# Optimization experiments

Hardware: AMD Instinct MI355X
Metric: run time of the kernel (lower is better)

Reference implementation:

```python
import jax, jax.numpy as jnp
import numpy as np

N = 50000
E = 800000
IN_C, HID_C, OUT_C = 128, 256, 2


def sage_conv(x, src, dst, W_l, b_l, W_r, num_nodes):
    # PyG SAGEConv with mean aggregation:
    #   out = lin_l(mean_{j in N(i)} x_j) + lin_r(x_i)
    msg = x[src]                                            # [E, d] gather
    agg = jax.ops.segment_sum(msg, dst, num_segments=num_nodes)   # [N, d]
    cnt = jax.ops.segment_sum(jnp.ones((msg.shape[0],), x.dtype), dst,
                              num_segments=num_nodes)        # [N]
    agg = agg / jnp.maximum(cnt, 1.0)[:, None]               # mean (deg>=1)
    return agg @ W_l.T + b_l + x @ W_r.T


def setup_inputs() -> dict:
    key = jax.random.key(0)
    ks = jax.random.split(key, 8)
    x = jax.random.normal(ks[0], (N, IN_C), dtype=jnp.float32)
    edge_index = jax.random.randint(ks[1], (2, E), 0, N, dtype=jnp.int32)
    # glorot-ish scaled params
    s1 = 1.0 / np.sqrt(IN_C)
    s2 = 1.0 / np.sqrt(HID_C)
    W1l = jax.random.normal(ks[2], (HID_C, IN_C), dtype=jnp.float32) * s1
    W1r = jax.random.normal(ks[3], (HID_C, IN_C), dtype=jnp.float32) * s1
    b1 = jnp.zeros((HID_C,), dtype=jnp.float32)
    W2l = jax.random.normal(ks[4], (OUT_C, HID_C), dtype=jnp.float32) * s2
    W2r = jax.random.normal(ks[5], (OUT_C, HID_C), dtype=jnp.float32) * s2
    b2 = jnp.zeros((OUT_C,), dtype=jnp.float32)
    return {"x": x, "edge_index": edge_index,
            "W1l": W1l, "b1": b1, "W1r": W1r,
            "W2l": W2l, "b2": b2, "W2r": W2r}


def reference(x, edge_index, W1l, b1, W1r, W2l, b2, W2r):
    src, dst = edge_index[0], edge_index[1]
    h = sage_conv(x, src, dst, W1l, b1, W1r, N)
    h = jax.nn.relu(h)
    out = sage_conv(h, src, dst, W2l, b2, W2r, N)
    return out
```

## Files before the change

### kernel.cpp

```cpp
#include <hip/hip_runtime.h>
#include <hip/hip_bf16.h>


#define IN_C 128
#define HID_C 256
#define BKT_SHIFT 7
#define BKT_W 128
#define CAP 3072

typedef __attribute__((ext_vector_type(8))) short short8;
typedef __attribute__((ext_vector_type(4))) float f32x4;

static __device__ __forceinline__ unsigned short f2b(float f) {
    __hip_bfloat16 h = __float2bfloat16(f);
    return *(unsigned short*)&h;
}
static __device__ __forceinline__ float b2f(unsigned short u) {
    unsigned v = ((unsigned)u) << 16;
    return *(float*)&v;
}

__global__ __launch_bounds__(512) void scatter_conv(
    const float* __restrict__ x, unsigned int* __restrict__ Abf,
    const float* __restrict__ w1l, const float* __restrict__ w1r,
    unsigned short* __restrict__ Bg,
    const int* __restrict__ ei, int* __restrict__ bcnt,
    unsigned int* __restrict__ binned,
    int nquads , int xblk, int E_) {
    __shared__ int hist[512];
    __shared__ int lbase[512];
    const int tid = threadIdx.x;
    if (blockIdx.x < xblk) {
        int t = blockIdx.x * 512 + tid;
        if (t >= nquads) return;
        float4 v = *(const float4*)&x[(size_t)t * 4];
        uint2 o;
        o.x = ((unsigned)f2b(v.y) << 16) | f2b(v.x);
        o.y = ((unsigned)f2b(v.w) << 16) | f2b(v.z);
        int node = t >> 5, g = t & 31;
        *(uint2*)&Abf[(size_t)node * 128 + 64 + g * 2] = o;
    } else if (blockIdx.x < xblk + 32) {
        int idx4 = (blockIdx.x - xblk) * 512 + tid;
        int o = idx4 >> 6, k4 = (idx4 & 63) * 4;
        const float* srcp = (k4 < IN_C) ? &w1l[o * IN_C + k4]
                                        : &w1r[o * IN_C + (k4 - IN_C)];
        float4 f = *(const float4*)srcp;
        ushort4 s;
        s.x = f2b(f.x); s.y = f2b(f.y); s.z = f2b(f.z); s.w = f2b(f.w);
        *(ushort4*)&Bg[(size_t)idx4 * 4] = s;
    } else {
        const int e0 = (blockIdx.x - xblk - 32) * 2048;
        hist[tid] = 0;
        __syncthreads();
        int dreg[4];
#pragma unroll
        for (int j = 0; j < 4; ++j) {
            int e = e0 + j * 512 + tid;
            dreg[j] = (e < E_) ? ei[E_ + e] : -1;
            if (dreg[j] >= 0) atomicAdd(&hist[dreg[j] >> BKT_SHIFT], 1);
        }
        __syncthreads();
        {
            int c = hist[tid];
            lbase[tid] = c ? tid * CAP + atomicAdd(&bcnt[tid], c) : 0;
            hist[tid] = 0;
        }
        __syncthreads();
#pragma unroll
        for (int j = 0; j < 4; ++j) {
            int e = e0 + j * 512 + tid;
            if (dreg[j] >= 0) {
                int d = dreg[j];
                int b = d >> BKT_SHIFT;
                int pos = lbase[b] + atomicAdd(&hist[b], 1);
                if (pos < b * CAP + CAP)
                    binned[pos] = ((unsigned)ei[e] << BKT_SHIFT) |
                                  (unsigned)(d & (BKT_W - 1));
            }
        }
    }
}


__global__ __launch_bounds__(1024) void sort_gather(
    unsigned int* __restrict__ binned, const int* __restrict__ bcnt,
    const uint4* __restrict__ abf4c, uint4* __restrict__ Abf4,
    int* __restrict__ deg, int* __restrict__ boffs, int n) {
    __shared__ unsigned int ebuf[CAP];
    __shared__ unsigned short sbuf[CAP];
    __shared__ int hist[BKT_W];
    __shared__ int offs[BKT_W];
    __shared__ int cur[BKT_W];
    const int tid = threadIdx.x;
    const int lane = tid & 63;
    const int bkt = blockIdx.x;
    const int gbase = bkt * CAP;
    int cnt = bcnt[bkt];
    if (cnt > CAP) cnt = CAP;

    if (tid < BKT_W) hist[tid] = 0;
    {
        const int cnt4 = cnt >> 2;
        const uint4* b4 = (const uint4*)(binned + gbase);
        uint4* e4 = (uint4*)ebuf;
        for (int i = tid; i < cnt4; i += 1024) e4[i] = b4[i];
        for (int i = cnt4 * 4 + tid; i < cnt; i += 1024)
            ebuf[i] = binned[gbase + i];
    }
    __syncthreads();
    for (int i = tid; i < cnt; i += 1024)
        atomicAdd(&hist[ebuf[i] & (BKT_W - 1)], 1);
    __syncthreads();
    if (tid < 64) {
        int h0 = hist[lane * 2], h1 = hist[lane * 2 + 1];
        int s = h0 + h1;
        int incl = s;
#pragma unroll
        for (int off = 1; off < 64; off <<= 1) {
            int t = __shfl_up(incl, off);
            if (lane >= off) incl += t;
        }
        int excl = incl - s;
        offs[lane * 2] = excl;          cur[lane * 2] = excl;
        offs[lane * 2 + 1] = excl + h0; cur[lane * 2 + 1] = excl + h0;
    }
    __syncthreads();
    for (int i = tid; i < cnt; i += 1024) {
        unsigned int pk = ebuf[i];
        int pos = atomicAdd(&cur[pk & (BKT_W - 1)], 1);
        sbuf[pos] = (unsigned short)(pk >> BKT_SHIFT);
    }
    if (tid < BKT_W) {
        int node = bkt * BKT_W + tid;
        if (node < n) { deg[node] = hist[tid]; boffs[node] = offs[tid]; }
    }
    __syncthreads();

    {
        unsigned int* so = (unsigned int*)(binned + gbase);
        const int half = (cnt + 1) >> 1;
        for (int i = tid; i < half; i += 1024) {
            unsigned lo = sbuf[i * 2];
            unsigned hi = (i * 2 + 1 < cnt) ? sbuf[i * 2 + 1] : 0u;
            so[i] = lo | (hi << 16);
        }
    }

    const int wv = tid >> 6;
    const int ep = lane >> 4;
    const int pos = lane & 15;
    for (int ld = wv * 8; ld < wv * 8 + 8; ++ld) {
        int node = bkt * BKT_W + ld;
        if (node >= n) break;
        int beg = offs[ld], end = offs[ld] + hist[ld];
        float s[8] = {0.f, 0.f, 0.f, 0.f, 0.f, 0.f, 0.f, 0.f};
        for (int e = beg; e < end; e += 16) {
#pragma unroll
            for (int g = 0; g < 4; ++g) {
                int eg = e + g * 4 + ep;
                if (eg < end) {
                    int src = sbuf[eg];
                    uint4 u = abf4c[(size_t)src * 32 + 16 + pos];
                    s[0] += b2f(u.x & 0xffff); s[1] += b2f(u.x >> 16);
                    s[2] += b2f(u.y & 0xffff); s[3] += b2f(u.y >> 16);
                    s[4] += b2f(u.z & 0xffff); s[5] += b2f(u.z >> 16);
                    s[6] += b2f(u.w & 0xffff); s[7] += b2f(u.w >> 16);
                }
            }
        }
#pragma unroll
        for (int i = 0; i < 8; ++i) {
            s[i] += __shfl_xor(s[i], 16);
            s[i] += __shfl_xor(s[i], 32);
        }
        if (ep == 0) {
            float inv = 1.0f / (float)max(end - beg, 1);
            uint4 o;
            o.x = ((unsigned)f2b(s[1] * inv) << 16) | f2b(s[0] * inv);
            o.y = ((unsigned)f2b(s[3] * inv) << 16) | f2b(s[2] * inv);
            o.z = ((unsigned)f2b(s[5] * inv) << 16) | f2b(s[4] * inv);
            o.w = ((unsigned)f2b(s[7] * inv) << 16) | f2b(s[6] * inv);
            Abf4[(size_t)node * 32 + pos] = o;
        }
    }
}


#define LSTR 72

__global__ __launch_bounds__(256, 4) void gemm1_fused(
    const unsigned short* __restrict__ Abf, const unsigned short* __restrict__ Bg,
    const float* __restrict__ b1, const float* __restrict__ w2l,
    const float* __restrict__ w2r, float2* __restrict__ p2g,
    float2* __restrict__ rsg, int nn) {
    __shared__ short Bs[256 * LSTR];

    const int tid = threadIdx.x;
    const int lane = tid & 63;
    const int wn = tid >> 6;
    const int row0 = blockIdx.x * 64;
    const int quad = lane >> 4;
    const int l16 = lane & 15;

    const unsigned short* ap[4];
#pragma unroll
    for (int mt = 0; mt < 4; ++mt) {
        int ar = row0 + mt * 16 + l16;
        if (ar >= nn) ar = nn - 1;
        ap[mt] = Abf + (size_t)ar * 256 + quad * 8;
    }

    f32x4 acc[4][4];
#pragma unroll
    for (int i = 0; i < 4; ++i)
#pragma unroll
        for (int j = 0; j < 4; ++j) acc[i][j] = (f32x4){0.f, 0.f, 0.f, 0.f};

    for (int k0 = 0; k0 < 256; k0 += 64) {
        const uint4* gb = (const uint4*)(Bg + (size_t)tid * 256 + k0);
        uint4 r0 = gb[0], r1 = gb[1], r2 = gb[2], r3 = gb[3];
        uint4 r4 = gb[4], r5 = gb[5], r6 = gb[6], r7 = gb[7];
        __syncthreads();
        uint4* lb = (uint4*)&Bs[tid * LSTR];
        lb[0] = r0; lb[1] = r1; lb[2] = r2; lb[3] = r3;
        lb[4] = r4; lb[5] = r5; lb[6] = r6; lb[7] = r7;
        __syncthreads();

#pragma unroll
        for (int kb = 0; kb < 2; ++kb) {
            short8 af[4], bf[4];
#pragma unroll
            for (int mt = 0; mt < 4; ++mt)
                af[mt] = *(const short8*)(ap[mt] + k0 + kb * 32);
#pragma unroll
            for (int nt = 0; nt < 4; ++nt)
                bf[nt] = *(const short8*)&Bs[(wn * 64 + nt * 16 + l16) * LSTR + kb * 32 + quad * 8];
#pragma unroll
            for (int mt = 0; mt < 4; ++mt)
#pragma unroll
                for (int nt = 0; nt < 4; ++nt)
                    acc[mt][nt] = __builtin_amdgcn_mfma_f32_16x16x32_bf16(
                        af[mt], bf[nt], acc[mt][nt], 0, 0, 0);
        }
    }

    float* pr = (float*)Bs;
    __syncthreads();
    pr[tid] = 0.f;
    __syncthreads();

    const int cbase = wn * 64 + l16;
#pragma unroll
    for (int half = 0; half < 2; ++half) {
        const float* wA = half ? w2r : w2l;
        f32x4 part[2][4];
#pragma unroll
        for (int c = 0; c < 2; ++c)
#pragma unroll
            for (int mt = 0; mt < 4; ++mt) part[c][mt] = (f32x4){0.f, 0.f, 0.f, 0.f};
#pragma unroll
        for (int nt = 0; nt < 4; ++nt) {
            const int col = cbase + nt * 16;
            const float bias = b1[col];
            const float w0 = wA[col];
            const float w1 = wA[HID_C + col];
#pragma unroll
            for (int mt = 0; mt < 4; ++mt)
#pragma unroll
                for (int r = 0; r < 4; ++r) {
                    float hv = fmaxf(acc[mt][nt][r] + bias, 0.0f);
                    part[0][mt][r] += hv * w0;
                    part[1][mt][r] += hv * w1;
                }
        }
#pragma unroll
        for (int c = 0; c < 2; ++c)
#pragma unroll
            for (int mt = 0; mt < 4; ++mt)
#pragma unroll
                for (int r = 0; r < 4; ++r)
#pragma unroll
                    for (int m = 1; m < 16; m <<= 1)
                        part[c][mt][r] += __shfl_xor(part[c][mt][r], m);
        if (l16 < 8) {
            const int ch2 = l16 & 1;
            const int mts = l16 >> 1;
#pragma unroll
            for (int r = 0; r < 4; ++r) {
                int rloc = quad * 4 + mts * 16 + r;
                atomicAdd(&pr[rloc * 4 + half * 2 + ch2], part[ch2][mts][r]);
            }
        }
    }
    __syncthreads();
    if (tid < 128) {
        int rloc = tid >> 1, pair = tid & 1;
        int row = row0 + rloc;
        if (row < nn) {
            float2 v = make_float2(pr[rloc * 4 + pair * 2],
                                   pr[rloc * 4 + pair * 2 + 1]);
            if (pair) rsg[row] = v; else p2g[row] = v;
        }
    }
}


__global__ __launch_bounds__(512) void fin_bucket(
    const unsigned int* __restrict__ binned, const int* __restrict__ boffs,
    const int* __restrict__ deg,
    const float2* __restrict__ p2, const float2* __restrict__ rs,
    const float* __restrict__ b2, float* __restrict__ out, int n) {
    __shared__ float ps0[3][BKT_W];
    __shared__ float ps1[3][BKT_W];
    const int tid = threadIdx.x;
    const int ln = tid & (BKT_W - 1);
    const int hp = tid >> 7;
    const int bkt = blockIdx.x;
    const int node = bkt * BKT_W + ln;
    const unsigned short* sp =
        (const unsigned short*)(binned + (size_t)bkt * CAP);
    float s0 = 0.f, s1 = 0.f;
    int dg = 0;
    if (node < n) {
        int beg = boffs[node];
        dg = deg[node];
        int end = beg + dg;
        for (int i = beg + hp; i < end; i += 4) {
            float2 v = p2[sp[i]];
            s0 += v.x; s1 += v.y;
        }
    }
    if (hp) { ps0[hp - 1][ln] = s0; ps1[hp - 1][ln] = s1; }
    __syncthreads();
    if (!hp && node < n) {
        s0 += ps0[0][ln] + ps0[1][ln] + ps0[2][ln];
        s1 += ps1[0][ln] + ps1[1][ln] + ps1[2][ln];
        float inv = 1.0f / (float)max(dg, 1);
        float2 self = rs[node];
        out[node * 2 + 0] = s0 * inv + self.x + b2[0];
        out[node * 2 + 1] = s1 * inv + self.y + b2[1];
    }
}


extern "C" void kernel_launch(void* const* d_in, const int* in_sizes, int n_in,
                              void* d_out, int out_size, void* d_ws, size_t ws_size,
                              hipStream_t stream) {
    const float* x   = (const float*)d_in[0];
    const int*   ei  = (const int*)d_in[1];
    const float* W1l = (const float*)d_in[2];
    const float* b1  = (const float*)d_in[3];
    const float* W1r = (const float*)d_in[4];
    const float* W2l = (const float*)d_in[5];
    const float* b2  = (const float*)d_in[6];
    const float* W2r = (const float*)d_in[7];
    float* out = (float*)d_out;

    const int N_ = in_sizes[0] / IN_C;
    const int E_ = in_sizes[1] / 2;
    const int nbkt = (N_ + BKT_W - 1) / BKT_W;

    char* wsb = (char*)d_ws;
    size_t off = 0;
    auto alloc = [&](size_t bytes) {
        void* ptr = wsb + off;
        off += ((bytes + 15) & ~(size_t)15);
        return ptr;
    };
    unsigned short* Abf = (unsigned short*)alloc((size_t)N_ * 256 * 2);
    unsigned short* Bg  = (unsigned short*)alloc(256 * 256 * 2);
    unsigned int* binned = (unsigned int*)alloc((size_t)(nbkt + 1) * CAP * 4);
    int*   bcnt = (int*)alloc(512 * 4);
    float* p2f  = (float*)alloc((size_t)N_ * 2 * 4);
    float* rsf  = (float*)alloc((size_t)N_ * 2 * 4);
    int*   deg  = (int*)alloc((size_t)N_ * 4);
    int*   boffs = (int*)alloc((size_t)N_ * 4);

    const int xblk = (N_ * 32 + 511) / 512;
    const int eblk = (E_ + 2047) / 2048;

    hipMemsetAsync(bcnt, 0, 512 * sizeof(int), stream);

    scatter_conv<<<xblk + 32 + eblk, 512, 0, stream>>>(
        x, (unsigned int*)Abf, W1l, W1r, Bg, ei, bcnt, binned,
        N_ * 32, xblk, E_);

    sort_gather<<<nbkt, 1024, 0, stream>>>(binned, bcnt, (const uint4*)Abf,
                                           (uint4*)Abf, deg, boffs, N_);

    gemm1_fused<<<(N_ + 63) / 64, 256, 0, stream>>>(
        Abf, Bg, b1, W2l, W2r, (float2*)p2f, (float2*)rsf, N_);

    fin_bucket<<<nbkt, 512, 0, stream>>>(binned, boffs, deg,
                                         (const float2*)p2f, (const float2*)rsf,
                                         b2, out, N_);
}
```

Before: 213.6 us.

## Retile fused GEMM into 128x128 blocks with shared-memory A staging and split N

The fused layer-1 GEMM moves from 64-row blocks that hold the whole 256-column B in LDS and read A straight from global memory to 128x128 tiles. Both A and B are staged through LDS, and the grid is split over two column halves. Each column half writes its own partial layer-2 projections, and the final kernel sums the two partials per node. This is meant to improve A reuse and load coalescing, at the cost of redundant A loads across the y-blocks, doubled partial buffers, and an extra gather per edge in the final aggregation.

```diff
diff --git a/kernel.cpp b/kernel.cpp
--- a/kernel.cpp
+++ b/kernel.cpp
@@ -188,42 +188,48 @@
 
 #define LSTR 72
 
-__global__ __launch_bounds__(256, 4) void gemm1_fused(
+__global__ __launch_bounds__(256) void gemm1_fused(
     const unsigned short* __restrict__ Abf, const unsigned short* __restrict__ Bg,
     const float* __restrict__ b1, const float* __restrict__ w2l,
     const float* __restrict__ w2r, float2* __restrict__ p2g,
     float2* __restrict__ rsg, int nn) {
-    __shared__ short Bs[256 * LSTR];
+    __shared__ short As[128 * LSTR];
+    __shared__ short Bs[128 * LSTR];
 
     const int tid = threadIdx.x;
     const int lane = tid & 63;
-    const int wn = tid >> 6;
-    const int row0 = blockIdx.x * 64;
+    const int wid = tid >> 6;
+    const int wm = wid >> 1, wn = wid & 1;
+    const int row0 = blockIdx.x * 128;
+    const int col0 = blockIdx.y * 128;
+
+    const int srow = tid >> 1;
+    const int skc = (tid & 1) * 32;
+    int arow = row0 + srow;
+    if (arow >= nn) arow = nn - 1;
+    const size_t agoff = (size_t)arow * 256 + skc;
+    const size_t bgoff = (size_t)(col0 + srow) * 256 + skc;
+
+    f32x4 acc[4][4];
+#pragma unroll
+    for (int i = 0; i < 4; ++i)
+#pragma unroll
+        for (int j = 0; j < 4; ++j) acc[i][j] = (f32x4){0.f, 0.f, 0.f, 0.f};
+
     const int quad = lane >> 4;
     const int l16 = lane & 15;
 
-    const unsigned short* ap[4];
-#pragma unroll
-    for (int mt = 0; mt < 4; ++mt) {
-        int ar = row0 + mt * 16 + l16;
-        if (ar >= nn) ar = nn - 1;
-        ap[mt] = Abf + (size_t)ar * 256 + quad * 8;
-    }
-
-    f32x4 acc[4][4];
-#pragma unroll
-    for (int i = 0; i < 4; ++i)
-#pragma unroll
-        for (int j = 0; j < 4; ++j) acc[i][j] = (f32x4){0.f, 0.f, 0.f, 0.f};
-
     for (int k0 = 0; k0 < 256; k0 += 64) {
-        const uint4* gb = (const uint4*)(Bg + (size_t)tid * 256 + k0);
-        uint4 r0 = gb[0], r1 = gb[1], r2 = gb[2], r3 = gb[3];
-        uint4 r4 = gb[4], r5 = gb[5], r6 = gb[6], r7 = gb[7];
+        const uint4* ga = (const uint4*)(Abf + agoff + k0);
+        const uint4* gb = (const uint4*)(Bg + bgoff + k0);
+        uint4 va0 = ga[0], va1 = ga[1], va2 = ga[2], va3 = ga[3];
+        uint4 vb0 = gb[0], vb1 = gb[1], vb2 = gb[2], vb3 = gb[3];
+
         __syncthreads();
-        uint4* lb = (uint4*)&Bs[tid * LSTR];
-        lb[0] = r0; lb[1] = r1; lb[2] = r2; lb[3] = r3;
-        lb[4] = r4; lb[5] = r5; lb[6] = r6; lb[7] = r7;
+        uint4* la = (uint4*)&As[srow * LSTR + skc];
+        uint4* lb = (uint4*)&Bs[srow * LSTR + skc];
+        la[0] = va0; la[1] = va1; la[2] = va2; la[3] = va3;
+        lb[0] = vb0; lb[1] = vb1; lb[2] = vb2; lb[3] = vb3;
         __syncthreads();
 
 #pragma unroll
@@ -231,7 +237,7 @@
             short8 af[4], bf[4];
 #pragma unroll
             for (int mt = 0; mt < 4; ++mt)
-                af[mt] = *(const short8*)(ap[mt] + k0 + kb * 32);
+                af[mt] = *(const short8*)&As[(wm * 64 + mt * 16 + l16) * LSTR + kb * 32 + quad * 8];
 #pragma unroll
             for (int nt = 0; nt < 4; ++nt)
                 bf[nt] = *(const short8*)&Bs[(wn * 64 + nt * 16 + l16) * LSTR + kb * 32 + quad * 8];
@@ -244,12 +250,12 @@
         }
     }
 
-    float* pr = (float*)Bs;
-    __syncthreads();
-    pr[tid] = 0.f;
-    __syncthreads();
-
-    const int cbase = wn * 64 + l16;
+    float* pr = (float*)As;
+    __syncthreads();
+    pr[tid] = 0.f; pr[tid + 256] = 0.f;
+    __syncthreads();
+
+    const int cbase = col0 + wn * 64 + l16;
 #pragma unroll
     for (int half = 0; half < 2; ++half) {
         const float* wA = half ? w2r : w2l;
@@ -287,19 +293,20 @@
             const int mts = l16 >> 1;
 #pragma unroll
             for (int r = 0; r < 4; ++r) {
-                int rloc = quad * 4 + mts * 16 + r;
+                int rloc = wm * 64 + quad * 4 + mts * 16 + r;
                 atomicAdd(&pr[rloc * 4 + half * 2 + ch2], part[ch2][mts][r]);
             }
         }
     }
     __syncthreads();
-    if (tid < 128) {
+    if (tid < 256) {
         int rloc = tid >> 1, pair = tid & 1;
         int row = row0 + rloc;
         if (row < nn) {
             float2 v = make_float2(pr[rloc * 4 + pair * 2],
                                    pr[rloc * 4 + pair * 2 + 1]);
-            if (pair) rsg[row] = v; else p2g[row] = v;
+            size_t idx = (size_t)blockIdx.y * nn + row;
+            if (pair) rsg[idx] = v; else p2g[idx] = v;
         }
     }
 }
@@ -326,8 +333,10 @@
         dg = deg[node];
         int end = beg + dg;
         for (int i = beg + hp; i < end; i += 4) {
-            float2 v = p2[sp[i]];
-            s0 += v.x; s1 += v.y;
+            int s = sp[i];
+            float2 va = p2[s];
+            float2 vb = p2[n + s];
+            s0 += va.x + vb.x; s1 += va.y + vb.y;
         }
     }
     if (hp) { ps0[hp - 1][ln] = s0; ps1[hp - 1][ln] = s1; }
@@ -336,9 +345,9 @@
         s0 += ps0[0][ln] + ps0[1][ln] + ps0[2][ln];
         s1 += ps1[0][ln] + ps1[1][ln] + ps1[2][ln];
         float inv = 1.0f / (float)max(dg, 1);
-        float2 self = rs[node];
-        out[node * 2 + 0] = s0 * inv + self.x + b2[0];
-        out[node * 2 + 1] = s1 * inv + self.y + b2[1];
+        float2 sa = rs[node], sb = rs[n + node];
+        out[node * 2 + 0] = s0 * inv + sa.x + sb.x + b2[0];
+        out[node * 2 + 1] = s1 * inv + sa.y + sb.y + b2[1];
     }
 }
 
@@ -371,8 +380,8 @@
     unsigned short* Bg  = (unsigned short*)alloc(256 * 256 * 2);
     unsigned int* binned = (unsigned int*)alloc((size_t)(nbkt + 1) * CAP * 4);
     int*   bcnt = (int*)alloc(512 * 4);
-    float* p2f  = (float*)alloc((size_t)N_ * 2 * 4);
-    float* rsf  = (float*)alloc((size_t)N_ * 2 * 4);
+    float* p2f  = (float*)alloc((size_t)N_ * 2 * 2 * 4);
+    float* rsf  = (float*)alloc((size_t)N_ * 2 * 2 * 4);
     int*   deg  = (int*)alloc((size_t)N_ * 4);
     int*   boffs = (int*)alloc((size_t)N_ * 4);
 
@@ -388,7 +397,7 @@
     sort_gather<<<nbkt, 1024, 0, stream>>>(binned, bcnt, (const uint4*)Abf,
                                            (uint4*)Abf, deg, boffs, N_);
 
-    gemm1_fused<<<(N_ + 63) / 64, 256, 0, stream>>>(
+    gemm1_fused<<<dim3((N_ + 127) / 128, 2), 256, 0, stream>>>(
         Abf, Bg, b1, W2l, W2r, (float2*)p2f, (float2*)rsf, N_);
 
     fin_bucket<<<nbkt, 512, 0, stream>>>(binned, boffs, deg,
```

Result: faster. 178.5 us (median of 2 runs) (-16.5%).
